# Kernel optimization log

Measured on AMD Instinct MI355X. Metric: run time of the kernel, lower is better.

## Reference

```python
import jax, jax.numpy as jnp
import numpy as np

K_TOP = 256  # top-k tokens selected per sample (init kwarg k)
LN_EPS = 1e-5


def _layer_norm(x, w, b, eps=LN_EPS):
    # LayerNorm over last dim (channels), biased variance as in torch
    m = x.mean(-1, keepdims=True)
    v = x.var(-1, keepdims=True)
    return (x - m) / jnp.sqrt(v + eps) * w + b


def setup_inputs() -> dict:
    key = jax.random.key(0)
    ks = jax.random.split(key, 5)
    B, C, H, W = 16, 512, 48, 48
    s = 1.0 / np.sqrt(C)
    x = jax.random.normal(ks[0], (B, C, H, W), jnp.float32)
    wq = jax.random.normal(ks[1], (C, C), jnp.float32) * s
    wk = jax.random.normal(ks[2], (C, C), jnp.float32) * s
    wv = jax.random.normal(ks[3], (C, C), jnp.float32) * s
    wo = jax.random.normal(ks[4], (C, C), jnp.float32) * s
    ln_w = jnp.ones((C,), jnp.float32)
    ln_b = jnp.zeros((C,), jnp.float32)
    return {"x": x, "wq": wq, "wk": wk, "wv": wv, "wo": wo, "ln_w": ln_w, "ln_b": ln_b}


def reference(x, wq, wk, wv, wo, ln_w, ln_b):
    B, C, H, W = x.shape
    N = H * W
    k_actual = min(K_TOP, N)
    scale = C ** (-0.5)

    xf = x.reshape(B, C, N)
    # 1x1 convs == per-token channel GEMMs
    q = jnp.einsum('oc,bcn->bon', wq, xf)
    kk = jnp.einsum('oc,bcn->bon', wk, xf)
    v = jnp.einsum('oc,bcn->bon', wv, xf)

    # L2 energy per token -> top-k selection
    importance = jnp.nan_to_num(jnp.sum(xf * xf, axis=1), nan=0.0, posinf=0.0, neginf=0.0)  # [B, N]
    _, topk_idx = jax.lax.top_k(importance, k_actual)  # [B, k]

    idx = topk_idx[:, None, :]  # [B, 1, k]
    q_sel = jnp.take_along_axis(q, jnp.broadcast_to(idx, (B, C, k_actual)), axis=2).transpose(0, 2, 1)  # [B, k, C]
    k_sel = jnp.take_along_axis(kk, jnp.broadcast_to(idx, (B, C, k_actual)), axis=2).transpose(0, 2, 1)
    v_sel = jnpp_take = jnp.take_along_axis(v, jnp.broadcast_to(idx, (B, C, k_actual)), axis=2).transpose(0, 2, 1)

    q_sel = _layer_norm(q_sel, ln_w, ln_b)
    k_sel = _layer_norm(k_sel, ln_w, ln_b)

    attn = jnp.einsum('bic,bjc->bij', q_sel, k_sel) * scale  # [B, k, k]
    attn = jnp.nan_to_num(attn, nan=0.0, posinf=0.0, neginf=0.0)
    attn = jnp.clip(attn, -80.0, 80.0)
    attn = jax.nn.softmax(attn, axis=-1)  # (internally max-subtracted, matches original)
    attn = jnp.nan_to_num(attn, nan=0.0, posinf=0.0, neginf=0.0)

    attended = jnp.einsum('bij,bjc->bic', attn, v_sel)  # [B, k, C]

    # scatter attended tokens back into v (non-selected tokens keep v values)
    bi = jnp.arange(B)[:, None, None]
    ci = jnp.arange(C)[None, :, None]
    out = v.at[bi, ci, idx].set(attended.transpose(0, 2, 1))  # [B, C, N]

    out = jnp.einsum('oc,bcn->bon', wo, out).reshape(B, C, H, W)
    return x + out
```

## Files before the change

kernel.cpp:

```cpp
#include <hip/hip_runtime.h>
#include <hip/hip_bf16.h>

#define BB   16
#define CC   512
#define NN   2304
#define KK   256
#define LNEPS 1e-5f
#define SCALE 0.04419417382415922f

typedef unsigned int  u32;
typedef unsigned short u16;
typedef __attribute__((ext_vector_type(8))) short short8;
typedef __attribute__((ext_vector_type(4))) float f32x4;

__device__ __forceinline__ u32 f2bf_u(float f) {
    u32 u = __float_as_uint(f);
    return (u + 0x7fffu + ((u >> 16) & 1u)) >> 16;
}
__device__ __forceinline__ u32 packf(float f) {
    u32 h = f2bf_u(f);
    float hf = __uint_as_float(h << 16);
    u32 l = f2bf_u(f - hf);
    return h | (l << 16);
}
__device__ __forceinline__ float unpackf(u32 p) {
    return __uint_as_float(p << 16) + __uint_as_float(p & 0xffff0000u);
}

__device__ __forceinline__ void gl16(const void* g, void* l) {
    __builtin_amdgcn_global_load_lds((const __attribute__((address_space(1))) u32*)g,
                                     (__attribute__((address_space(3))) u32*)l, 16, 0, 0);
}

__global__ __launch_bounds__(256) void importance_kernel(const float* __restrict__ X,
                                                         float* __restrict__ imp) {
    int b = blockIdx.x / 9;
    int n = (blockIdx.x % 9) * 256 + threadIdx.x;
    const float* xp = X + (size_t)b * CC * NN + n;
    double s = 0.0;
    #pragma unroll 8
    for (int c = 0; c < CC; ++c) {
        float v = xp[(size_t)c * NN];
        s = fma((double)v, (double)v, s);
    }
    imp[b * NN + n] = (float)s;
}

__global__ __launch_bounds__(1024) void topk_kernel(const float* __restrict__ imp,
                                                    int* __restrict__ idx) {
    __shared__ unsigned long long keys[4096];
    const int b = blockIdx.x, tid = threadIdx.x;
    for (int i = tid; i < 4096; i += 1024) {
        unsigned long long kv = 0ULL;
        if (i < NN) {
            unsigned u = __float_as_uint(imp[b * NN + i]);
            u = (u & 0x80000000u) ? ~u : (u | 0x80000000u);
            kv = ((unsigned long long)u << 32) | (unsigned)(NN - 1 - i);
        }
        keys[i] = kv;
    }
    __syncthreads();
    for (int k = 2; k <= 4096; k <<= 1) {
        for (int j = k >> 1; j > 0; j >>= 1) {
            for (int i = tid; i < 4096; i += 1024) {
                int l = i ^ j;
                if (l > i) {
                    unsigned long long a = keys[i], c = keys[l];
                    bool desc = ((i & k) == 0);
                    if (desc ? (a < c) : (a > c)) { keys[i] = c; keys[l] = a; }
                }
            }
            __syncthreads();
        }
    }
    if (tid < KK) idx[b * KK + tid] = NN - 1 - (int)(keys[tid] & 0xffffffffu);
}

__global__ __launch_bounds__(256) void transpose_cvt(const float* __restrict__ X,
                                                     u32* __restrict__ XT) {
    __shared__ u32 T[64 * 65];
    const int b = blockIdx.z;
    const int n0 = blockIdx.x * 64, c0 = blockIdx.y * 64;
    const int t = threadIdx.x;
    const int cl = t >> 4, nl4 = (t & 15) * 4;
    #pragma unroll
    for (int p = 0; p < 4; ++p) {
        int c = cl + 16 * p;
        float4 v = *(const float4*)&X[((size_t)(b * CC + c0 + c)) * NN + n0 + nl4];
        T[c * 65 + nl4 + 0] = packf(v.x);
        T[c * 65 + nl4 + 1] = packf(v.y);
        T[c * 65 + nl4 + 2] = packf(v.z);
        T[c * 65 + nl4 + 3] = packf(v.w);
    }
    __syncthreads();
    const int cch = t & 15;
    #pragma unroll
    for (int q = 0; q < 4; ++q) {
        int n = (t >> 4) + 16 * q;
        uint4 o;
        o.x = T[(cch * 4 + 0) * 65 + n];
        o.y = T[(cch * 4 + 1) * 65 + n];
        o.z = T[(cch * 4 + 2) * 65 + n];
        o.w = T[(cch * 4 + 3) * 65 + n];
        *(uint4*)&XT[((size_t)b * NN + n0 + n) * CC + c0 + cch * 4] = o;
    }
}

__global__ __launch_bounds__(256) void cvt_w(const float* __restrict__ W,
                                             u16* __restrict__ Wh, u16* __restrict__ Wl) {
    int i4 = (blockIdx.x * 256 + threadIdx.x) * 4;
    float4 v = *(const float4*)&W[i4];
    ushort4 h, l;
    h.x = (u16)f2bf_u(v.x); l.x = (u16)f2bf_u(v.x - __uint_as_float((u32)h.x << 16));
    h.y = (u16)f2bf_u(v.y); l.y = (u16)f2bf_u(v.y - __uint_as_float((u32)h.y << 16));
    h.z = (u16)f2bf_u(v.z); l.z = (u16)f2bf_u(v.z - __uint_as_float((u32)h.z << 16));
    h.w = (u16)f2bf_u(v.w); l.w = (u16)f2bf_u(v.w - __uint_as_float((u32)h.w << 16));
    *(ushort4*)&Wh[i4] = h;
    *(ushort4*)&Wl[i4] = l;
}

template<int EPI>
__global__ __launch_bounds__(256) void mfma_gemm(
    const u16* __restrict__ Ah, const u16* __restrict__ Al,
    const u32* __restrict__ Bpk, long sBb, int nbN,
    const int* __restrict__ rowidx,
    const float* __restrict__ Xres,
    void* __restrict__ Yv, long sYb)
{
    __shared__ u16 sAh[128 * 32];
    __shared__ u16 sAl[128 * 32];
    __shared__ u32 sB[128 * 32];
    const int lin = blockIdx.x;
    const int xcd = lin & 7, slot = (lin >> 3) & 3, grp = lin >> 5;
    const int p = grp * 8 + xcd;
    const int b = p / nbN, nb = p - b * nbN;
    const int n0 = nb * 128;
    const int c0 = slot * 128;
    const int t = threadIdx.x;
    const int wid = t >> 6, lane = t & 63;
    const int mw = (wid >> 1) * 64, nw = (wid & 1) * 64;
    const int lm = lane & 15, lk = lane >> 4;
    const u32* Bb = Bpk + (size_t)b * sBb;

    size_t brow[4];
    #pragma unroll
    for (int i = 0; i < 4; ++i) {
        int r = (t >> 3) + 32 * i;
        int gr = rowidx ? rowidx[b * KK + n0 + r] : (n0 + r);
        brow[i] = (size_t)gr * CC;
    }

    f32x4 acc[4][4] = {};

    for (int k0 = 0; k0 < 512; k0 += 32) {
        #pragma unroll
        for (int i = 0; i < 2; ++i) {
            int e = t + 256 * i, r = e >> 2, ch = e & 3;
            int gch = ch ^ (r & 3);
            gl16(&Ah[(size_t)(c0 + r) * 512 + k0 + gch * 8], &sAh[e * 8]);
            gl16(&Al[(size_t)(c0 + r) * 512 + k0 + gch * 8], &sAl[e * 8]);
        }
        #pragma unroll
        for (int i = 0; i < 4; ++i) {
            int e = t + 256 * i, ch = e & 7;
            int r = (t >> 3) + 32 * i;
            int gch = ch ^ (r & 7);
            gl16(&Bb[brow[i] + k0 + gch * 4], &sB[e * 4]);
        }
        __syncthreads();

        short8 ah[4], al[4], bh[4], bl[4];
        #pragma unroll
        for (int i = 0; i < 4; ++i) {
            int m = mw + 16 * i + lm;
            int ach = lk ^ (m & 3);
            ah[i] = *(const short8*)&sAh[m * 32 + ach * 8];
            al[i] = *(const short8*)&sAl[m * 32 + ach * 8];
        }
        #pragma unroll
        for (int j = 0; j < 4; ++j) {
            int n = nw + 16 * j + lm;
            const u32* prow = &sB[n * 32];
            int ca = (2 * lk) ^ (n & 7);
            int cb = (2 * lk + 1) ^ (n & 7);
            uint4 u0 = *(const uint4*)&prow[ca * 4];
            uint4 u1 = *(const uint4*)&prow[cb * 4];
            union { u32 u[4]; short8 s; } H, L;
            H.u[0] = __builtin_amdgcn_perm(u0.y, u0.x, 0x05040100u);
            H.u[1] = __builtin_amdgcn_perm(u0.w, u0.z, 0x05040100u);
            H.u[2] = __builtin_amdgcn_perm(u1.y, u1.x, 0x05040100u);
            H.u[3] = __builtin_amdgcn_perm(u1.w, u1.z, 0x05040100u);
            L.u[0] = __builtin_amdgcn_perm(u0.y, u0.x, 0x07060302u);
            L.u[1] = __builtin_amdgcn_perm(u0.w, u0.z, 0x07060302u);
            L.u[2] = __builtin_amdgcn_perm(u1.y, u1.x, 0x07060302u);
            L.u[3] = __builtin_amdgcn_perm(u1.w, u1.z, 0x07060302u);
            bh[j] = H.s; bl[j] = L.s;
        }
        #pragma unroll
        for (int i = 0; i < 4; ++i)
            #pragma unroll
            for (int j = 0; j < 4; ++j) {
                acc[i][j] = __builtin_amdgcn_mfma_f32_16x16x32_bf16(ah[i], bh[j], acc[i][j], 0, 0, 0);
                acc[i][j] = __builtin_amdgcn_mfma_f32_16x16x32_bf16(ah[i], bl[j], acc[i][j], 0, 0, 0);
                acc[i][j] = __builtin_amdgcn_mfma_f32_16x16x32_bf16(al[i], bh[j], acc[i][j], 0, 0, 0);
            }
        __syncthreads();
    }

    if (EPI == 0) {
        u32* Y = (u32*)Yv + (size_t)b * sYb;
        #pragma unroll
        for (int i = 0; i < 4; ++i)
            #pragma unroll
            for (int j = 0; j < 4; ++j) {
                uint4 o;
                o.x = packf(acc[i][j][0]);
                o.y = packf(acc[i][j][1]);
                o.z = packf(acc[i][j][2]);
                o.w = packf(acc[i][j][3]);
                *(uint4*)&Y[(size_t)(n0 + nw + 16 * j + lm) * CC + c0 + mw + 16 * i + 4 * lk] = o;
            }
    } else {
        float* Y = (float*)Yv + (size_t)b * sYb;
        const float* Xb = Xres + (size_t)b * sYb;
        #pragma unroll
        for (int i = 0; i < 4; ++i)
            #pragma unroll
            for (int r = 0; r < 4; ++r) {
                size_t roff = (size_t)(c0 + mw + 16 * i + 4 * lk + r) * NN;
                #pragma unroll
                for (int j = 0; j < 4; ++j) {
                    size_t off = roff + n0 + nw + 16 * j + lm;
                    Y[off] = acc[i][j][r] + Xb[off];
                }
            }
    }
}

template<bool BT, bool RES, bool SC, bool YT>
__global__ __launch_bounds__(256) void tile_gemm(
    const float* __restrict__ A, long sAb, int lda,
    const float* __restrict__ Bm, long sBb, int ldb,
    const float* __restrict__ R, long sRb,
    float* __restrict__ Y, long sYb, int ldy,
    int Kd, float scalev)
{
    __shared__ float At[16][68];
    __shared__ float Bt[16][68];
    const int b  = blockIdx.z;
    const int n0 = blockIdx.x * 64;
    const int m0 = blockIdx.y * 64;
    const int tid = threadIdx.x;
    const int ti = tid >> 4, tj = tid & 15;
    const int arow = tid >> 2, akk = (tid & 3) << 2;
    const int bkk  = tid >> 4, bjx = (tid & 15) << 2;
    const float* Ab = A  + (size_t)b * sAb;
    const float* Bb = Bm + (size_t)b * sBb;
    float acc[4][4] = {{0.f}};

    for (int k0 = 0; k0 < Kd; k0 += 16) {
        float4 a4 = *(const float4*)&Ab[(size_t)(m0 + arow) * lda + k0 + akk];
        At[akk + 0][arow] = a4.x; At[akk + 1][arow] = a4.y;
        At[akk + 2][arow] = a4.z; At[akk + 3][arow] = a4.w;
        if (BT) {
            float4 b4 = *(const float4*)&Bb[(size_t)(n0 + arow) * ldb + k0 + akk];
            Bt[akk + 0][arow] = b4.x; Bt[akk + 1][arow] = b4.y;
            Bt[akk + 2][arow] = b4.z; Bt[akk + 3][arow] = b4.w;
        } else {
            *(float4*)&Bt[bkk][bjx] = *(const float4*)&Bb[(size_t)(k0 + bkk) * ldb + n0 + bjx];
        }
        __syncthreads();
        #pragma unroll
        for (int kk = 0; kk < 16; ++kk) {
            const float4 av = *(const float4*)&At[kk][ti * 4];
            const float4 bv = *(const float4*)&Bt[kk][tj * 4];
            const float ar[4] = {av.x, av.y, av.z, av.w};
            const float br[4] = {bv.x, bv.y, bv.z, bv.w};
            #pragma unroll
            for (int r = 0; r < 4; ++r)
                #pragma unroll
                for (int c = 0; c < 4; ++c)
                    acc[r][c] += ar[r] * br[c];
        }
        __syncthreads();
    }

    float* Yb = Y + (size_t)b * sYb;
    if (YT) {
        #pragma unroll
        for (int c = 0; c < 4; ++c) {
            float4 o4 = make_float4(acc[0][c], acc[1][c], acc[2][c], acc[3][c]);
            *(float4*)&Yb[(size_t)(n0 + tj * 4 + c) * ldy + (m0 + ti * 4)] = o4;
        }
    } else {
        const float* Rb = RES ? (R + (size_t)b * sRb) : nullptr;
        #pragma unroll
        for (int r = 0; r < 4; ++r) {
            float4 o4 = make_float4(acc[r][0], acc[r][1], acc[r][2], acc[r][3]);
            if (SC) {
                o4.x = fminf(fmaxf(o4.x * scalev, -80.f), 80.f);
                o4.y = fminf(fmaxf(o4.y * scalev, -80.f), 80.f);
                o4.z = fminf(fmaxf(o4.z * scalev, -80.f), 80.f);
                o4.w = fminf(fmaxf(o4.w * scalev, -80.f), 80.f);
            }
            size_t off = (size_t)(m0 + ti * 4 + r) * ldy + n0 + tj * 4;
            if (RES) {
                float4 r4 = *(const float4*)&Rb[off];
                o4.x += r4.x; o4.y += r4.y; o4.z += r4.z; o4.w += r4.w;
            }
            *(float4*)&Yb[off] = o4;
        }
    }
}

__global__ __launch_bounds__(256) void ln_rows_packed(u32* __restrict__ P,
                                                      const float* __restrict__ lnw,
                                                      const float* __restrict__ lnb) {
    const int wave = threadIdx.x >> 6, lane = threadIdx.x & 63;
    const int row = blockIdx.x * 4 + wave;
    u32* p = P + (size_t)row * CC;
    uint4 ua = *(uint4*)&p[lane * 4];
    uint4 ub = *(uint4*)&p[256 + lane * 4];
    float4 v0 = make_float4(unpackf(ua.x), unpackf(ua.y), unpackf(ua.z), unpackf(ua.w));
    float4 v1 = make_float4(unpackf(ub.x), unpackf(ub.y), unpackf(ub.z), unpackf(ub.w));
    float s  = v0.x + v0.y + v0.z + v0.w + v1.x + v1.y + v1.z + v1.w;
    float s2 = v0.x*v0.x + v0.y*v0.y + v0.z*v0.z + v0.w*v0.w
             + v1.x*v1.x + v1.y*v1.y + v1.z*v1.z + v1.w*v1.w;
    #pragma unroll
    for (int m = 32; m >= 1; m >>= 1) { s += __shfl_xor(s, m); s2 += __shfl_xor(s2, m); }
    const float mean = s * (1.f / 512.f);
    const float var  = s2 * (1.f / 512.f) - mean * mean;
    const float rstd = rsqrtf(var + LNEPS);
    float4 w0 = *(const float4*)&lnw[lane * 4],        b0 = *(const float4*)&lnb[lane * 4];
    float4 w1 = *(const float4*)&lnw[256 + lane * 4],  b1 = *(const float4*)&lnb[256 + lane * 4];
    v0.x = (v0.x - mean) * rstd * w0.x + b0.x;  v0.y = (v0.y - mean) * rstd * w0.y + b0.y;
    v0.z = (v0.z - mean) * rstd * w0.z + b0.z;  v0.w = (v0.w - mean) * rstd * w0.w + b0.w;
    v1.x = (v1.x - mean) * rstd * w1.x + b1.x;  v1.y = (v1.y - mean) * rstd * w1.y + b1.y;
    v1.z = (v1.z - mean) * rstd * w1.z + b1.z;  v1.w = (v1.w - mean) * rstd * w1.w + b1.w;
    float* q = (float*)p;
    *(float4*)&q[lane * 4] = v0;
    *(float4*)&q[256 + lane * 4] = v1;
}

__global__ __launch_bounds__(256) void softmax_rows(float* __restrict__ S) {
    const int wave = threadIdx.x >> 6, lane = threadIdx.x & 63;
    const int row = blockIdx.x * 4 + wave;
    float* p = S + (size_t)row * KK;
    float4 v = *(float4*)&p[lane * 4];
    float m = fmaxf(fmaxf(v.x, v.y), fmaxf(v.z, v.w));
    #pragma unroll
    for (int mk = 32; mk >= 1; mk >>= 1) m = fmaxf(m, __shfl_xor(m, mk));
    float4 e = make_float4(expf(v.x - m), expf(v.y - m), expf(v.z - m), expf(v.w - m));
    float s = e.x + e.y + e.z + e.w;
    #pragma unroll
    for (int mk = 32; mk >= 1; mk >>= 1) s += __shfl_xor(s, mk);
    const float inv = 1.f / s;
    e.x *= inv; e.y *= inv; e.z *= inv; e.w *= inv;
    *(float4*)&p[lane * 4] = e;
}

__global__ __launch_bounds__(256) void gather_vsel(const u32* __restrict__ VT,
                                                   const int* __restrict__ idx,
                                                   float* __restrict__ Vsel) {
    const int wave = threadIdx.x >> 6, lane = threadIdx.x & 63;
    const int gj = blockIdx.x * 4 + wave;
    const int b = gj >> 8, j = gj & 255;
    const int n = idx[b * KK + j];
    const u32* vp = VT + ((size_t)b * NN + n) * CC;
    float* op = Vsel + (size_t)gj * CC;
    uint4 ua = *(const uint4*)&vp[lane * 8];
    uint4 ub = *(const uint4*)&vp[lane * 8 + 4];
    float4 fa = make_float4(unpackf(ua.x), unpackf(ua.y), unpackf(ua.z), unpackf(ua.w));
    float4 fb = make_float4(unpackf(ub.x), unpackf(ub.y), unpackf(ub.z), unpackf(ub.w));
    *(float4*)&op[lane * 8] = fa;
    *(float4*)&op[lane * 8 + 4] = fb;
}

__global__ __launch_bounds__(256) void scatter_att(const float* __restrict__ Att,
                                                   const int* __restrict__ idx,
                                                   u32* __restrict__ VT) {
    const int wave = threadIdx.x >> 6, lane = threadIdx.x & 63;
    const int gi = blockIdx.x * 4 + wave;
    const int b = gi >> 8, i = gi & 255;
    const int n = idx[b * KK + i];
    const float* ap = Att + (size_t)gi * CC;
    u32* vp = VT + ((size_t)b * NN + n) * CC;
    float4 fa = *(const float4*)&ap[lane * 8];
    float4 fb = *(const float4*)&ap[lane * 8 + 4];
    uint4 ua, ub;
    ua.x = packf(fa.x); ua.y = packf(fa.y); ua.z = packf(fa.z); ua.w = packf(fa.w);
    ub.x = packf(fb.x); ub.y = packf(fb.y); ub.z = packf(fb.z); ub.w = packf(fb.w);
    *(uint4*)&vp[lane * 8] = ua;
    *(uint4*)&vp[lane * 8 + 4] = ub;
}

extern "C" void kernel_launch(void* const* d_in, const int* in_sizes, int n_in,
                              void* d_out, int out_size, void* d_ws, size_t ws_size,
                              hipStream_t stream) {
    const float* x   = (const float*)d_in[0];
    const float* wq  = (const float*)d_in[1];
    const float* wk  = (const float*)d_in[2];
    const float* wv  = (const float*)d_in[3];
    const float* wo  = (const float*)d_in[4];
    const float* lnw = (const float*)d_in[5];
    const float* lnb = (const float*)d_in[6];
    float* out = (float*)d_out;

    char* w = (char*)d_ws;
    int*   idx   = (int*)w;
    float* imp   = (float*)(w + 16384);
    float* att   = imp;
    u32*   qbufP = (u32*)(w + 8404992);
    u32*   kbufP = (u32*)(w + 16793600);
    float* S     = (float*)(w + 25182208);
    float* vsel  = (float*)(w + 29376512);
    u32*   vbufT = (u32*)(w + 37765120);
    u16* WvH = (u16*)qbufP;  u16* WvL = WvH + 262144;
    u16* WoH = (u16*)kbufP;  u16* WoL = WoH + 262144;
    u16* WqH = (u16*)vsel;   u16* WqL = WqH + 262144;
    u16* WkH = WqH + 524288; u16* WkL = WqH + 786432;
    u32* XT  = (u32*)d_out;
    float* qbuf = (float*)qbufP;
    float* kbuf = (float*)kbufP;

    const long sXp = (long)NN * CC;
    const long sQp = (long)KK * CC;
    const long sQ  = (long)KK * CC;
    const long sS  = (long)KK * KK;

    importance_kernel<<<dim3(BB * 9), dim3(256), 0, stream>>>(x, imp);
    topk_kernel<<<dim3(BB), dim3(1024), 0, stream>>>(imp, idx);

    cvt_w<<<dim3(256), dim3(256), 0, stream>>>(wv, WvH, WvL);
    cvt_w<<<dim3(256), dim3(256), 0, stream>>>(wq, WqH, WqL);
    cvt_w<<<dim3(256), dim3(256), 0, stream>>>(wk, WkH, WkL);
    transpose_cvt<<<dim3(NN / 64, CC / 64, BB), dim3(256), 0, stream>>>(x, XT);

    mfma_gemm<0><<<dim3(18 * 4 * BB), dim3(256), 0, stream>>>(
        WvH, WvL, XT, sXp, 18, nullptr, nullptr, (void*)vbufT, sXp);

    mfma_gemm<0><<<dim3(2 * 4 * BB), dim3(256), 0, stream>>>(
        WqH, WqL, XT, sXp, 2, idx, nullptr, (void*)qbufP, sQp);
    mfma_gemm<0><<<dim3(2 * 4 * BB), dim3(256), 0, stream>>>(
        WkH, WkL, XT, sXp, 2, idx, nullptr, (void*)kbufP, sQp);

    ln_rows_packed<<<dim3(BB * KK / 4), dim3(256), 0, stream>>>(qbufP, lnw, lnb);
    ln_rows_packed<<<dim3(BB * KK / 4), dim3(256), 0, stream>>>(kbufP, lnw, lnb);

    tile_gemm<true,false,true,false><<<dim3(KK/64, KK/64, BB), dim3(256), 0, stream>>>(
        qbuf, sQ, CC, kbuf, sQ, CC, nullptr, 0, S, sS, KK, CC, SCALE);
    softmax_rows<<<dim3(BB * KK / 4), dim3(256), 0, stream>>>(S);

    gather_vsel<<<dim3(BB * KK / 4), dim3(256), 0, stream>>>(vbufT, idx, vsel);
    tile_gemm<false,false,false,false><<<dim3(CC/64, KK/64, BB), dim3(256), 0, stream>>>(
        S, sS, KK, vsel, sQ, CC, nullptr, 0, att, sQ, CC, KK, 1.f);
    scatter_att<<<dim3(BB * KK / 4), dim3(256), 0, stream>>>(att, idx, vbufT);

    cvt_w<<<dim3(256), dim3(256), 0, stream>>>(wo, WoH, WoL);
    mfma_gemm<1><<<dim3(18 * 4 * BB), dim3(256), 0, stream>>>(
        WoH, WoL, vbufT, sXp, 18, nullptr, x, (void*)out, (long)CC * NN);
}
```

Measured before the change: 531.3 us.

## Double-buffer LDS tiles in MFMA GEMM to overlap loads with compute

Doubles the shared-memory tiles for A (hi/lo) and packed B, and restructures the k-loop so the next tile's async global-to-LDS loads are issued before computing on the current tile. This removes one barrier per iteration and is meant to hide global load latency behind MFMA work. In exchange, LDS use per block doubles to about 64KB, which may reduce occupancy. It also relies on gl16 completion being ordered correctly by the barrier.

```diff
diff --git a/kernel.cpp b/kernel.cpp
--- a/kernel.cpp
+++ b/kernel.cpp
@@ -127,9 +127,9 @@
     const float* __restrict__ Xres,
     void* __restrict__ Yv, long sYb)
 {
-    __shared__ u16 sAh[128 * 32];
-    __shared__ u16 sAl[128 * 32];
-    __shared__ u32 sB[128 * 32];
+    __shared__ u16 sAh[2][128 * 32];
+    __shared__ u16 sAl[2][128 * 32];
+    __shared__ u32 sB[2][128 * 32];
     const int lin = blockIdx.x;
     const int xcd = lin & 7, slot = (lin >> 3) & 3, grp = lin >> 5;
     const int p = grp * 8 + xcd;
@@ -152,35 +152,36 @@
 
     f32x4 acc[4][4] = {};
 
-    for (int k0 = 0; k0 < 512; k0 += 32) {
+    auto STAGE = [&](int buf, int k0) {
         #pragma unroll
         for (int i = 0; i < 2; ++i) {
             int e = t + 256 * i, r = e >> 2, ch = e & 3;
             int gch = ch ^ (r & 3);
-            gl16(&Ah[(size_t)(c0 + r) * 512 + k0 + gch * 8], &sAh[e * 8]);
-            gl16(&Al[(size_t)(c0 + r) * 512 + k0 + gch * 8], &sAl[e * 8]);
+            gl16(&Ah[(size_t)(c0 + r) * 512 + k0 + gch * 8], &sAh[buf][e * 8]);
+            gl16(&Al[(size_t)(c0 + r) * 512 + k0 + gch * 8], &sAl[buf][e * 8]);
         }
         #pragma unroll
         for (int i = 0; i < 4; ++i) {
             int e = t + 256 * i, ch = e & 7;
             int r = (t >> 3) + 32 * i;
             int gch = ch ^ (r & 7);
-            gl16(&Bb[brow[i] + k0 + gch * 4], &sB[e * 4]);
-        }
-        __syncthreads();
-
+            gl16(&Bb[brow[i] + k0 + gch * 4], &sB[buf][e * 4]);
+        }
+    };
+
+    auto COMPUTE = [&](int buf) {
         short8 ah[4], al[4], bh[4], bl[4];
         #pragma unroll
         for (int i = 0; i < 4; ++i) {
             int m = mw + 16 * i + lm;
             int ach = lk ^ (m & 3);
-            ah[i] = *(const short8*)&sAh[m * 32 + ach * 8];
-            al[i] = *(const short8*)&sAl[m * 32 + ach * 8];
+            ah[i] = *(const short8*)&sAh[buf][m * 32 + ach * 8];
+            al[i] = *(const short8*)&sAl[buf][m * 32 + ach * 8];
         }
         #pragma unroll
         for (int j = 0; j < 4; ++j) {
             int n = nw + 16 * j + lm;
-            const u32* prow = &sB[n * 32];
+            const u32* prow = &sB[buf][n * 32];
             int ca = (2 * lk) ^ (n & 7);
             int cb = (2 * lk + 1) ^ (n & 7);
             uint4 u0 = *(const uint4*)&prow[ca * 4];
@@ -204,6 +205,16 @@
                 acc[i][j] = __builtin_amdgcn_mfma_f32_16x16x32_bf16(ah[i], bl[j], acc[i][j], 0, 0, 0);
                 acc[i][j] = __builtin_amdgcn_mfma_f32_16x16x32_bf16(al[i], bh[j], acc[i][j], 0, 0, 0);
             }
+    };
+
+    STAGE(0, 0);
+    __syncthreads();
+    for (int ks = 0; ks < 16; ks += 2) {
+        STAGE(1, (ks + 1) * 32);
+        COMPUTE(0);
+        __syncthreads();
+        if (ks < 14) STAGE(0, (ks + 2) * 32);
+        COMPUTE(1);
         __syncthreads();
     }
 
```

After: 527.1 us. Within noise of the previous version (-0.8%).

## Fuse importance into transpose, batch weight conversions, and move QK^T to MFMA

Applied to the files above, without the earlier changes.

Computes per-token L2 energy inside the transpose/convert kernel using double atomics, which removes the separate strided pass over x. Merges the three weight conversions into one launch and the Q and K projection GEMMs into one launch. Also merges the two LayerNorm launches and keeps LayerNorm output in packed bf16 hi/lo form. The attention score GEMM moves from the fp32 tile GEMM to the split-bf16 MFMA GEMM with a fused scale and clip epilogue. It also drops the XCD-aware block swizzle in favour of a 3D grid, which may change L2 locality, and it adds a memset plus atomics.

```diff
diff --git a/kernel.cpp b/kernel.cpp
--- a/kernel.cpp
+++ b/kernel.cpp
@@ -32,57 +32,16 @@
                                      (__attribute__((address_space(3))) u32*)l, 16, 0, 0);
 }
 
-__global__ __launch_bounds__(256) void importance_kernel(const float* __restrict__ X,
-                                                         float* __restrict__ imp) {
-    int b = blockIdx.x / 9;
-    int n = (blockIdx.x % 9) * 256 + threadIdx.x;
-    const float* xp = X + (size_t)b * CC * NN + n;
-    double s = 0.0;
-    #pragma unroll 8
-    for (int c = 0; c < CC; ++c) {
-        float v = xp[(size_t)c * NN];
-        s = fma((double)v, (double)v, s);
-    }
-    imp[b * NN + n] = (float)s;
-}
-
-__global__ __launch_bounds__(1024) void topk_kernel(const float* __restrict__ imp,
-                                                    int* __restrict__ idx) {
-    __shared__ unsigned long long keys[4096];
-    const int b = blockIdx.x, tid = threadIdx.x;
-    for (int i = tid; i < 4096; i += 1024) {
-        unsigned long long kv = 0ULL;
-        if (i < NN) {
-            unsigned u = __float_as_uint(imp[b * NN + i]);
-            u = (u & 0x80000000u) ? ~u : (u | 0x80000000u);
-            kv = ((unsigned long long)u << 32) | (unsigned)(NN - 1 - i);
-        }
-        keys[i] = kv;
-    }
-    __syncthreads();
-    for (int k = 2; k <= 4096; k <<= 1) {
-        for (int j = k >> 1; j > 0; j >>= 1) {
-            for (int i = tid; i < 4096; i += 1024) {
-                int l = i ^ j;
-                if (l > i) {
-                    unsigned long long a = keys[i], c = keys[l];
-                    bool desc = ((i & k) == 0);
-                    if (desc ? (a < c) : (a > c)) { keys[i] = c; keys[l] = a; }
-                }
-            }
-            __syncthreads();
-        }
-    }
-    if (tid < KK) idx[b * KK + tid] = NN - 1 - (int)(keys[tid] & 0xffffffffu);
-}
-
-__global__ __launch_bounds__(256) void transpose_cvt(const float* __restrict__ X,
-                                                     u32* __restrict__ XT) {
+__global__ __launch_bounds__(256) void transpose_imp(const float* __restrict__ X,
+                                                     u32* __restrict__ XT,
+                                                     double* __restrict__ impd) {
     __shared__ u32 T[64 * 65];
+    __shared__ double S2[16][65];
     const int b = blockIdx.z;
     const int n0 = blockIdx.x * 64, c0 = blockIdx.y * 64;
     const int t = threadIdx.x;
     const int cl = t >> 4, nl4 = (t & 15) * 4;
+    double p0 = 0.0, p1 = 0.0, p2 = 0.0, p3 = 0.0;
     #pragma unroll
     for (int p = 0; p < 4; ++p) {
         int c = cl + 16 * p;
@@ -91,7 +50,15 @@
         T[c * 65 + nl4 + 1] = packf(v.y);
         T[c * 65 + nl4 + 2] = packf(v.z);
         T[c * 65 + nl4 + 3] = packf(v.w);
-    }
+        p0 += (double)v.x * v.x;
+        p1 += (double)v.y * v.y;
+        p2 += (double)v.z * v.z;
+        p3 += (double)v.w * v.w;
+    }
+    S2[cl][nl4 + 0] = p0;
+    S2[cl][nl4 + 1] = p1;
+    S2[cl][nl4 + 2] = p2;
+    S2[cl][nl4 + 3] = p3;
     __syncthreads();
     const int cch = t & 15;
     #pragma unroll
@@ -104,11 +71,46 @@
         o.w = T[(cch * 4 + 3) * 65 + n];
         *(uint4*)&XT[((size_t)b * NN + n0 + n) * CC + c0 + cch * 4] = o;
     }
-}
-
-__global__ __launch_bounds__(256) void cvt_w(const float* __restrict__ W,
-                                             u16* __restrict__ Wh, u16* __restrict__ Wl) {
-    int i4 = (blockIdx.x * 256 + threadIdx.x) * 4;
+    if (t < 64) {
+        double s = 0.0;
+        #pragma unroll
+        for (int c2 = 0; c2 < 16; ++c2) s += S2[c2][t];
+        atomicAdd(&impd[b * NN + n0 + t], s);
+    }
+}
+
+__global__ __launch_bounds__(1024) void topk_kernel(const double* __restrict__ impd,
+                                                    int* __restrict__ idx) {
+    __shared__ unsigned long long keys[4096];
+    const int b = blockIdx.x, tid = threadIdx.x;
+    for (int i = tid; i < 4096; i += 1024) {
+        unsigned long long kv = 0ULL;
+        if (i < NN) {
+            float fv = (float)impd[b * NN + i];
+            unsigned u = __float_as_uint(fv);
+            u = (u & 0x80000000u) ? ~u : (u | 0x80000000u);
+            kv = ((unsigned long long)u << 32) | (unsigned)(NN - 1 - i);
+        }
+        keys[i] = kv;
+    }
+    __syncthreads();
+    for (int k = 2; k <= 4096; k <<= 1) {
+        for (int j = k >> 1; j > 0; j >>= 1) {
+            for (int i = tid; i < 4096; i += 1024) {
+                int l = i ^ j;
+                if (l > i) {
+                    unsigned long long a = keys[i], c = keys[l];
+                    bool desc = ((i & k) == 0);
+                    if (desc ? (a < c) : (a > c)) { keys[i] = c; keys[l] = a; }
+                }
+            }
+            __syncthreads();
+        }
+    }
+    if (tid < KK) idx[b * KK + tid] = NN - 1 - (int)(keys[tid] & 0xffffffffu);
+}
+
+__device__ __forceinline__ void cvt_one(const float* W, u16* Wh, u16* Wl, int i4) {
     float4 v = *(const float4*)&W[i4];
     ushort4 h, l;
     h.x = (u16)f2bf_u(v.x); l.x = (u16)f2bf_u(v.x - __uint_as_float((u32)h.x << 16));
@@ -118,29 +120,52 @@
     *(ushort4*)&Wh[i4] = h;
     *(ushort4*)&Wl[i4] = l;
 }
-
-template<int EPI>
+__global__ __launch_bounds__(256) void cvt_w3(
+    const float* __restrict__ w0, const float* __restrict__ w1, const float* __restrict__ w2,
+    u16* __restrict__ h0, u16* __restrict__ l0,
+    u16* __restrict__ h1, u16* __restrict__ l1,
+    u16* __restrict__ h2, u16* __restrict__ l2) {
+    int wi = blockIdx.x >> 8;
+    int i4 = ((blockIdx.x & 255) * 256 + threadIdx.x) * 4;
+    const float* W = (wi == 0) ? w0 : (wi == 1) ? w1 : w2;
+    u16* Wh = (wi == 0) ? h0 : (wi == 1) ? h1 : h2;
+    u16* Wl = (wi == 0) ? l0 : (wi == 1) ? l1 : l2;
+    cvt_one(W, Wh, Wl, i4);
+}
+__global__ __launch_bounds__(256) void cvt_w(const float* __restrict__ W,
+                                             u16* __restrict__ Wh, u16* __restrict__ Wl) {
+    int i4 = (blockIdx.x * 256 + threadIdx.x) * 4;
+    cvt_one(W, Wh, Wl, i4);
+}
+
+template<int EPI, bool QKF, bool APK>
 __global__ __launch_bounds__(256) void mfma_gemm(
-    const u16* __restrict__ Ah, const u16* __restrict__ Al,
-    const u32* __restrict__ Bpk, long sBb, int nbN,
+    const void* A1h, const void* A1l,
+    const void* A2h, const void* A2l,
+    long sAb,
+    const u32* __restrict__ Bpk, long sBb,
     const int* __restrict__ rowidx,
     const float* __restrict__ Xres,
-    void* __restrict__ Yv, long sYb)
+    void* Yv, void* Yv2, long sYb, int ldy, float scalev)
 {
-    __shared__ u16 sAh[128 * 32];
-    __shared__ u16 sAl[128 * 32];
-    __shared__ u32 sB[128 * 32];
-    const int lin = blockIdx.x;
-    const int xcd = lin & 7, slot = (lin >> 3) & 3, grp = lin >> 5;
-    const int p = grp * 8 + xcd;
-    const int b = p / nbN, nb = p - b * nbN;
-    const int n0 = nb * 128;
-    const int c0 = slot * 128;
+    __shared__ u32 smem[8192];
+    u16* sAh  = (u16*)smem;
+    u16* sAl  = (u16*)(smem + 2048);
+    u32* sA32 = smem;
+    u32* sB   = smem + 4096;
+    const int gx  = blockIdx.x;
+    const int sel = QKF ? (gx >> 1) : 0;
+    const int n0  = QKF ? ((gx & 1) * 128) : (gx * 128);
+    const int c0  = blockIdx.y * 128;
+    const int b   = blockIdx.z;
     const int t = threadIdx.x;
     const int wid = t >> 6, lane = t & 63;
     const int mw = (wid >> 1) * 64, nw = (wid & 1) * 64;
     const int lm = lane & 15, lk = lane >> 4;
     const u32* Bb = Bpk + (size_t)b * sBb;
+    const u16* Ah = (const u16*)((QKF && sel) ? A2h : A1h);
+    const u16* Al = (const u16*)((QKF && sel) ? A2l : A1l);
+    const u32* Apk = (const u32*)A1h + (size_t)b * sAb;
 
     size_t brow[4];
     #pragma unroll
@@ -153,12 +178,21 @@
     f32x4 acc[4][4] = {};
 
     for (int k0 = 0; k0 < 512; k0 += 32) {
-        #pragma unroll
-        for (int i = 0; i < 2; ++i) {
-            int e = t + 256 * i, r = e >> 2, ch = e & 3;
-            int gch = ch ^ (r & 3);
-            gl16(&Ah[(size_t)(c0 + r) * 512 + k0 + gch * 8], &sAh[e * 8]);
-            gl16(&Al[(size_t)(c0 + r) * 512 + k0 + gch * 8], &sAl[e * 8]);
+        if constexpr (!APK) {
+            #pragma unroll
+            for (int i = 0; i < 2; ++i) {
+                int e = t + 256 * i, r = e >> 2, ch = e & 3;
+                int gch = ch ^ (r & 3);
+                gl16(&Ah[(size_t)(c0 + r) * 512 + k0 + gch * 8], &sAh[e * 8]);
+                gl16(&Al[(size_t)(c0 + r) * 512 + k0 + gch * 8], &sAl[e * 8]);
+            }
+        } else {
+            #pragma unroll
+            for (int i = 0; i < 4; ++i) {
+                int e = t + 256 * i, r = e >> 3, ch = e & 7;
+                int gch = ch ^ (r & 7);
+                gl16(&Apk[(size_t)(c0 + r) * 512 + k0 + gch * 4], &sA32[e * 4]);
+            }
         }
         #pragma unroll
         for (int i = 0; i < 4; ++i) {
@@ -173,9 +207,27 @@
         #pragma unroll
         for (int i = 0; i < 4; ++i) {
             int m = mw + 16 * i + lm;
-            int ach = lk ^ (m & 3);
-            ah[i] = *(const short8*)&sAh[m * 32 + ach * 8];
-            al[i] = *(const short8*)&sAl[m * 32 + ach * 8];
+            if constexpr (!APK) {
+                int ach = lk ^ (m & 3);
+                ah[i] = *(const short8*)&sAh[m * 32 + ach * 8];
+                al[i] = *(const short8*)&sAl[m * 32 + ach * 8];
+            } else {
+                const u32* pa = &sA32[m * 32];
+                int ca = (2 * lk) ^ (m & 7);
+                int cb = (2 * lk + 1) ^ (m & 7);
+                uint4 u0 = *(const uint4*)&pa[ca * 4];
+                uint4 u1 = *(const uint4*)&pa[cb * 4];
+                union { u32 u[4]; short8 s; } H, L;
+                H.u[0] = __builtin_amdgcn_perm(u0.y, u0.x, 0x05040100u);
+                H.u[1] = __builtin_amdgcn_perm(u0.w, u0.z, 0x05040100u);
+                H.u[2] = __builtin_amdgcn_perm(u1.y, u1.x, 0x05040100u);
+                H.u[3] = __builtin_amdgcn_perm(u1.w, u1.z, 0x05040100u);
+                L.u[0] = __builtin_amdgcn_perm(u0.y, u0.x, 0x07060302u);
+                L.u[1] = __builtin_amdgcn_perm(u0.w, u0.z, 0x07060302u);
+                L.u[2] = __builtin_amdgcn_perm(u1.y, u1.x, 0x07060302u);
+                L.u[3] = __builtin_amdgcn_perm(u1.w, u1.z, 0x07060302u);
+                ah[i] = H.s; al[i] = L.s;
+            }
         }
         #pragma unroll
         for (int j = 0; j < 4; ++j) {
@@ -208,7 +260,7 @@
     }
 
     if (EPI == 0) {
-        u32* Y = (u32*)Yv + (size_t)b * sYb;
+        u32* Y = (u32*)((QKF && sel) ? Yv2 : Yv) + (size_t)b * sYb;
         #pragma unroll
         for (int i = 0; i < 4; ++i)
             #pragma unroll
@@ -220,7 +272,7 @@
                 o.w = packf(acc[i][j][3]);
                 *(uint4*)&Y[(size_t)(n0 + nw + 16 * j + lm) * CC + c0 + mw + 16 * i + 4 * lk] = o;
             }
-    } else {
+    } else if (EPI == 1) {
         float* Y = (float*)Yv + (size_t)b * sYb;
         const float* Xb = Xres + (size_t)b * sYb;
         #pragma unroll
@@ -232,6 +284,20 @@
                 for (int j = 0; j < 4; ++j) {
                     size_t off = roff + n0 + nw + 16 * j + lm;
                     Y[off] = acc[i][j][r] + Xb[off];
+                }
+            }
+    } else {
+        float* Y = (float*)Yv + (size_t)b * sYb;
+        #pragma unroll
+        for (int i = 0; i < 4; ++i)
+            #pragma unroll
+            for (int r = 0; r < 4; ++r) {
+                size_t roff = (size_t)(c0 + mw + 16 * i + 4 * lk + r) * ldy;
+                #pragma unroll
+                for (int j = 0; j < 4; ++j) {
+                    float v = acc[i][j][r] * scalev;
+                    v = fminf(fmaxf(v, -80.f), 80.f);
+                    Y[roff + n0 + nw + 16 * j + lm] = v;
                 }
             }
     }
@@ -313,12 +379,15 @@
     }
 }
 
-__global__ __launch_bounds__(256) void ln_rows_packed(u32* __restrict__ P,
+__global__ __launch_bounds__(256) void ln_rows_packed(u32* __restrict__ Q,
+                                                      u32* __restrict__ Kb,
                                                       const float* __restrict__ lnw,
                                                       const float* __restrict__ lnb) {
     const int wave = threadIdx.x >> 6, lane = threadIdx.x & 63;
-    const int row = blockIdx.x * 4 + wave;
-    u32* p = P + (size_t)row * CC;
+    const int row_g = blockIdx.x * 4 + wave;
+    u32* base = (row_g < BB * KK) ? Q : Kb;
+    const int row = row_g & (BB * KK - 1);
+    u32* p = base + (size_t)row * CC;
     uint4 ua = *(uint4*)&p[lane * 4];
     uint4 ub = *(uint4*)&p[256 + lane * 4];
     float4 v0 = make_float4(unpackf(ua.x), unpackf(ua.y), unpackf(ua.z), unpackf(ua.w));
@@ -337,9 +406,10 @@
     v0.z = (v0.z - mean) * rstd * w0.z + b0.z;  v0.w = (v0.w - mean) * rstd * w0.w + b0.w;
     v1.x = (v1.x - mean) * rstd * w1.x + b1.x;  v1.y = (v1.y - mean) * rstd * w1.y + b1.y;
     v1.z = (v1.z - mean) * rstd * w1.z + b1.z;  v1.w = (v1.w - mean) * rstd * w1.w + b1.w;
-    float* q = (float*)p;
-    *(float4*)&q[lane * 4] = v0;
-    *(float4*)&q[256 + lane * 4] = v1;
+    ua.x = packf(v0.x); ua.y = packf(v0.y); ua.z = packf(v0.z); ua.w = packf(v0.w);
+    ub.x = packf(v1.x); ub.y = packf(v1.y); ub.z = packf(v1.z); ub.w = packf(v1.w);
+    *(uint4*)&p[lane * 4] = ua;
+    *(uint4*)&p[256 + lane * 4] = ub;
 }
 
 __global__ __launch_bounds__(256) void softmax_rows(float* __restrict__ S) {
@@ -407,48 +477,44 @@
     float* out = (float*)d_out;
 
     char* w = (char*)d_ws;
-    int*   idx   = (int*)w;
-    float* imp   = (float*)(w + 16384);
-    float* att   = imp;
-    u32*   qbufP = (u32*)(w + 8404992);
-    u32*   kbufP = (u32*)(w + 16793600);
-    float* S     = (float*)(w + 25182208);
-    float* vsel  = (float*)(w + 29376512);
-    u32*   vbufT = (u32*)(w + 37765120);
+    int*    idx   = (int*)w;
+    double* impd  = (double*)(w + 16384);
+    float*  att   = (float*)(w + 16384);
+    u32*    qbufP = (u32*)(w + 8404992);
+    u32*    kbufP = (u32*)(w + 16793600);
+    float*  S     = (float*)(w + 25182208);
+    float*  vsel  = (float*)(w + 29376512);
+    u32*    vbufT = (u32*)(w + 37765120);
     u16* WvH = (u16*)qbufP;  u16* WvL = WvH + 262144;
     u16* WoH = (u16*)kbufP;  u16* WoL = WoH + 262144;
     u16* WqH = (u16*)vsel;   u16* WqL = WqH + 262144;
     u16* WkH = WqH + 524288; u16* WkL = WqH + 786432;
     u32* XT  = (u32*)d_out;
-    float* qbuf = (float*)qbufP;
-    float* kbuf = (float*)kbufP;
 
     const long sXp = (long)NN * CC;
     const long sQp = (long)KK * CC;
     const long sQ  = (long)KK * CC;
     const long sS  = (long)KK * KK;
 
-    importance_kernel<<<dim3(BB * 9), dim3(256), 0, stream>>>(x, imp);
-    topk_kernel<<<dim3(BB), dim3(1024), 0, stream>>>(imp, idx);
-
-    cvt_w<<<dim3(256), dim3(256), 0, stream>>>(wv, WvH, WvL);
-    cvt_w<<<dim3(256), dim3(256), 0, stream>>>(wq, WqH, WqL);
-    cvt_w<<<dim3(256), dim3(256), 0, stream>>>(wk, WkH, WkL);
-    transpose_cvt<<<dim3(NN / 64, CC / 64, BB), dim3(256), 0, stream>>>(x, XT);
-
-    mfma_gemm<0><<<dim3(18 * 4 * BB), dim3(256), 0, stream>>>(
-        WvH, WvL, XT, sXp, 18, nullptr, nullptr, (void*)vbufT, sXp);
-
-    mfma_gemm<0><<<dim3(2 * 4 * BB), dim3(256), 0, stream>>>(
-        WqH, WqL, XT, sXp, 2, idx, nullptr, (void*)qbufP, sQp);
-    mfma_gemm<0><<<dim3(2 * 4 * BB), dim3(256), 0, stream>>>(
-        WkH, WkL, XT, sXp, 2, idx, nullptr, (void*)kbufP, sQp);
-
-    ln_rows_packed<<<dim3(BB * KK / 4), dim3(256), 0, stream>>>(qbufP, lnw, lnb);
-    ln_rows_packed<<<dim3(BB * KK / 4), dim3(256), 0, stream>>>(kbufP, lnw, lnb);
-
-    tile_gemm<true,false,true,false><<<dim3(KK/64, KK/64, BB), dim3(256), 0, stream>>>(
-        qbuf, sQ, CC, kbuf, sQ, CC, nullptr, 0, S, sS, KK, CC, SCALE);
+    hipMemsetAsync(impd, 0, (size_t)BB * NN * sizeof(double), stream);
+    transpose_imp<<<dim3(NN / 64, CC / 64, BB), dim3(256), 0, stream>>>(x, XT, impd);
+    topk_kernel<<<dim3(BB), dim3(1024), 0, stream>>>(impd, idx);
+
+    cvt_w3<<<dim3(768), dim3(256), 0, stream>>>(wv, wq, wk, WvH, WvL, WqH, WqL, WkH, WkL);
+
+    mfma_gemm<0, false, false><<<dim3(18, 4, BB), dim3(256), 0, stream>>>(
+        WvH, WvL, nullptr, nullptr, 0, XT, sXp, nullptr, nullptr,
+        (void*)vbufT, nullptr, sXp, 0, 1.f);
+
+    mfma_gemm<0, true, false><<<dim3(4, 4, BB), dim3(256), 0, stream>>>(
+        WqH, WqL, WkH, WkL, 0, XT, sXp, idx, nullptr,
+        (void*)qbufP, (void*)kbufP, sQp, 0, 1.f);
+
+    ln_rows_packed<<<dim3(2 * BB * KK / 4), dim3(256), 0, stream>>>(qbufP, kbufP, lnw, lnb);
+
+    mfma_gemm<2, false, true><<<dim3(2, 2, BB), dim3(256), 0, stream>>>(
+        qbufP, nullptr, nullptr, nullptr, sQp, kbufP, sQp, nullptr, nullptr,
+        (void*)S, nullptr, sS, KK, SCALE);
     softmax_rows<<<dim3(BB * KK / 4), dim3(256), 0, stream>>>(S);
 
     gather_vsel<<<dim3(BB * KK / 4), dim3(256), 0, stream>>>(vbufT, idx, vsel);
@@ -457,6 +523,7 @@
     scatter_att<<<dim3(BB * KK / 4), dim3(256), 0, stream>>>(att, idx, vbufT);
 
     cvt_w<<<dim3(256), dim3(256), 0, stream>>>(wo, WoH, WoL);
-    mfma_gemm<1><<<dim3(18 * 4 * BB), dim3(256), 0, stream>>>(
-        WoH, WoL, vbufT, sXp, 18, nullptr, x, (void*)out, (long)CC * NN);
-}
+    mfma_gemm<1, false, false><<<dim3(18, 4, BB), dim3(256), 0, stream>>>(
+        WoH, WoL, nullptr, nullptr, 0, vbufT, sXp, nullptr, x,
+        (void*)out, nullptr, (long)CC * NN, 0, 1.f);
+}
```

Result: faster. 507.0 us (-4.6%).
